# Optimization experiments

Hardware: AMD Instinct MI355X
Metric: run time of the kernel (lower is better)

Reference implementation:

```python
import jax, jax.numpy as jnp
import numpy as np

B, T, D, H, O = 256, 512, 128, 128, 64


def setup_inputs() -> dict:
    key = jax.random.key(0)
    ks = jax.random.split(key, 10)
    s = 1.0 / np.sqrt(H)
    u = lambda k, shape: jax.random.uniform(k, shape, jnp.float32, -s, s)
    return {
        "x": jax.random.normal(ks[0], (B, T, D), jnp.float32),
        "W_ih": u(ks[1], (4 * H, D)),   # torch gate order: i, f, g, o
        "W_hh": u(ks[2], (4 * H, H)),
        "b_ih": u(ks[3], (4 * H,)),
        "b_hh": u(ks[4], (4 * H,)),
        "W1": u(ks[5], (H, H)),
        "b1": u(ks[6], (H,)),
        "W2": u(ks[7], (O, H)),
        "b2": u(ks[8], (O,)),
    }


def lstm_scan(x, W_ih, W_hh, b_ih, b_hh):
    b, t, _ = x.shape
    h4 = W_hh.shape[0] // 4
    # precompute input contribution for all timesteps (one big GEMM)
    xg = jnp.einsum('btd,gd->btg', x, W_ih) + b_ih + b_hh  # (B,T,4H)
    xg = jnp.swapaxes(xg, 0, 1)  # (T,B,4H) for scan over time

    def step(carry, xg_t):
        h, c = carry
        g = xg_t + h @ W_hh.T  # (B,4H)
        i, f, gg, o = jnp.split(g, 4, axis=-1)
        i = jax.nn.sigmoid(i)
        f = jax.nn.sigmoid(f)
        gg = jnp.tanh(gg)
        o = jax.nn.sigmoid(o)
        c = f * c + i * gg
        h = o * jnp.tanh(c)
        return (h, c), h

    h0 = jnp.zeros((b, h4), x.dtype)
    c0 = jnp.zeros((b, h4), x.dtype)
    _, hs = jax.lax.scan(step, (h0, c0), xg)  # hs: (T,B,H)
    return jnp.swapaxes(hs, 0, 1)  # (B,T,H), matching torch batch_first


def reference(x, W_ih, W_hh, b_ih, b_hh, W1, b1, W2, b2):
    b, t, _ = x.shape
    h = lstm_scan(x, W_ih, W_hh, b_ih, b_hh)          # (B,T,H)
    hflat = h.reshape(-1, h.shape[-1])                 # (B*T,H), b-major (as torch)
    hflat = hflat @ W1.T + b1
    y = hflat @ W2.T + b2                              # (B*T,O)
    # faithful to original: reshape flattened b-major rows as (T,B,O), take [-1]
    y = y.reshape(t, b, -1)
    return y[-1]                                       # (B,O)
```

## Files before the change

kernel.cpp:

```cpp
#include <hip/hip_runtime.h>
#include <math.h>

#define BB 256
#define TT 512
#define DD 128
#define HH 128
#define GG 512
#define OO 64

#define LOG2E    1.44269504088896340736f
#define TWOLOG2E 2.88539008177792681472f

typedef _Float16 half8 __attribute__((ext_vector_type(8)));
typedef float    f32x4 __attribute__((ext_vector_type(4)));

__global__ __launch_bounds__(512) void xgpack_kernel(
    const float* __restrict__ x,
    const float* __restrict__ W_ih,
    const float* __restrict__ b_ih,
    const float* __restrict__ b_hh,
    const float* __restrict__ W_hh,
    float* __restrict__ xg,
    _Float16* __restrict__ Wp)
{
    if (blockIdx.x >= TT) {
        const int g = (blockIdx.x - TT) * 512 + threadIdx.x;
        const int fid = g >> 6, l = g & 63;
        const int w = fid >> 5, rem = fid & 31, nt = rem >> 2, kt = rem & 3;
        const int quad = l >> 4, col = l & 15;
        const int row = (nt >> 1) * 128 + (nt & 1) * 16 + w * 32 + col;
        const int off = kt * 32 + quad * 8;
        const float ws = ((row >> 7) == 2) ? TWOLOG2E : LOG2E;
        const float* s = W_hh + row * HH + off;
        _Float16* d = Wp + (size_t)g * 8;
#pragma unroll
        for (int i = 0; i < 8; i++) d[i] = (_Float16)(s[i] * ws);
        return;
    }

    const int t = blockIdx.x;
    const int g = threadIdx.x;

    __shared__ __align__(16) float xs[DD];
    if (g < DD) xs[g] = x[(255 * TT + t) * DD + g];
    __syncthreads();

    const float4* __restrict__ wrow = (const float4*)(W_ih + g * DD);
    const float4* __restrict__ xv   = (const float4*)xs;

    float a0 = 0.f, a1 = 0.f, a2 = 0.f, a3 = 0.f;
#pragma unroll
    for (int i = 0; i < DD / 4; i += 4) {
        float4 w0 = wrow[i + 0], w1 = wrow[i + 1], w2 = wrow[i + 2], w3 = wrow[i + 3];
        float4 h0 = xv[i + 0],  h1 = xv[i + 1],  h2 = xv[i + 2],  h3 = xv[i + 3];
        a0 += w0.x * h0.x + w0.y * h0.y + w0.z * h0.z + w0.w * h0.w;
        a1 += w1.x * h1.x + w1.y * h1.y + w1.z * h1.z + w1.w * h1.w;
        a2 += w2.x * h2.x + w2.y * h2.y + w2.z * h2.z + w2.w * h2.w;
        a3 += w3.x * h3.x + w3.y * h3.y + w3.z * h3.z + w3.w * h3.w;
    }
    const float scale = ((g >> 7) == 2) ? TWOLOG2E : LOG2E;
    const float val = ((a0 + a1) + (a2 + a3) + b_ih[g] + b_hh[g]) * scale;
    xg[t * GG + (g & 127) * 4 + (g >> 7)] = val;
}

__global__
__attribute__((amdgpu_flat_work_group_size(256, 256), amdgpu_waves_per_eu(1, 1)))
void scan_kernel(
    const _Float16* __restrict__ Wp,
    const float* __restrict__ xgp,
    float* __restrict__ hs)
{
    const int tid  = threadIdx.x;
    const int lane = tid & 63;
    const int w    = tid >> 6;
    const int col  = lane & 15;
    const int quad = lane >> 4;
    const int wbase = w * 32;
    const bool sel  = (lane >= 32);
    const int jsel  = wbase + (sel ? 16 : 0) + col;
    const int aoff  = quad * 8;
    const bool wr   = (quad == 0) || (quad == 3);

    __shared__ __align__(16) _Float16 h_lds[2][HH];
    __shared__ __align__(16) float hs_l[BB * HH];

#define BLOADP(nt, kt) \
    half8 B##nt##_##kt = *(const half8*)(Wp + (((w * 32 + (nt) * 4 + (kt)) * 64 + lane) * 8));
#define FOR_KT(X, nt) X(nt, 0) X(nt, 1) X(nt, 2) X(nt, 3)
#define FOR_NT(X) FOR_KT(X, 0) FOR_KT(X, 1) FOR_KT(X, 2) FOR_KT(X, 3) \
                  FOR_KT(X, 4) FOR_KT(X, 5) FOR_KT(X, 6) FOR_KT(X, 7)
    FOR_NT(BLOADP)

    asm volatile("" : "+v"(B0_0), "+v"(B0_1), "+v"(B0_2), "+v"(B0_3),
                      "+v"(B1_0), "+v"(B1_1), "+v"(B1_2), "+v"(B1_3),
                      "+v"(B2_0), "+v"(B2_1), "+v"(B2_2), "+v"(B2_3),
                      "+v"(B3_0), "+v"(B3_1), "+v"(B3_2), "+v"(B3_3));
    asm volatile("" : "+v"(B4_0), "+v"(B4_1), "+v"(B4_2), "+v"(B4_3),
                      "+v"(B5_0), "+v"(B5_1), "+v"(B5_2), "+v"(B5_3),
                      "+v"(B6_0), "+v"(B6_1), "+v"(B6_2), "+v"(B6_3),
                      "+v"(B7_0), "+v"(B7_1), "+v"(B7_2), "+v"(B7_3));

    if (tid < HH) h_lds[0][tid] = (_Float16)0.f;

    f32x4 Z = {0.f, 0.f, 0.f, 0.f};
    asm volatile("" : "+v"(Z));

    const float* __restrict__ xgl = xgp + jsel * 4;
    f32x4 xg0 = *(const f32x4*)(xgl + 0 * GG);
    f32x4 xg1 = *(const f32x4*)(xgl + 1 * GG);

    float c = 0.f;
    __syncthreads();

#define MM(a, b, cc) __builtin_amdgcn_mfma_f32_16x16x32_f16((a), (b), (cc), 0, 0, 0)
#define STEP(par, XCUR) do {                                                            \
    const int t = t2 + (par);                                                           \
    f32x4 xpf = *(const f32x4*)(xgl + ((t + 2) & (TT - 1)) * GG);                       \
    const _Float16* hl = h_lds[(par)];                                                  \
    half8 A0 = *(const half8*)(hl +  0 + aoff);                                         \
    half8 A1 = *(const half8*)(hl + 32 + aoff);                                         \
    half8 A2 = *(const half8*)(hl + 64 + aoff);                                         \
    half8 A3 = *(const half8*)(hl + 96 + aoff);                                         \
    f32x4 C0, C1, C2, C3, C4, C5, C6, C7;                                               \
    C4 = MM(A0, B4_0, Z);  C5 = MM(A0, B5_0, Z);  C0 = MM(A0, B0_0, Z);                 \
    C1 = MM(A0, B1_0, Z);  C2 = MM(A0, B2_0, Z);  C3 = MM(A0, B3_0, Z);                 \
    C6 = MM(A0, B6_0, Z);  C7 = MM(A0, B7_0, Z);                                        \
    C4 = MM(A1, B4_1, C4); C5 = MM(A1, B5_1, C5); C0 = MM(A1, B0_1, C0);                \
    C1 = MM(A1, B1_1, C1); C2 = MM(A1, B2_1, C2); C3 = MM(A1, B3_1, C3);                \
    C6 = MM(A1, B6_1, C6); C7 = MM(A1, B7_1, C7);                                       \
    C4 = MM(A2, B4_2, C4); C5 = MM(A2, B5_2, C5); C0 = MM(A2, B0_2, C0);                \
    C1 = MM(A2, B1_2, C1); C2 = MM(A2, B2_2, C2); C3 = MM(A2, B3_2, C3);                \
    C6 = MM(A2, B6_2, C6); C7 = MM(A2, B7_2, C7);                                       \
    C4 = MM(A3, B4_3, C4); C5 = MM(A3, B5_3, C5); C0 = MM(A3, B0_3, C0);                \
    C1 = MM(A3, B1_3, C1); C2 = MM(A3, B2_3, C2); C3 = MM(A3, B3_3, C3);                \
    C6 = MM(A3, B6_3, C6); C7 = MM(A3, B7_3, C7);                                       \
                   \
    float pi = (sel ? C1[0] : C0[0]) + (XCUR).x;                                        \
    float pf = (sel ? C3[0] : C2[0]) + (XCUR).y;                                        \
    float pg = (sel ? C5[0] : C4[0]) + (XCUR).z;                                        \
    float po = (sel ? C7[0] : C6[0]) + (XCUR).w;                                        \
    float iv = __builtin_amdgcn_rcpf(1.0f + __builtin_amdgcn_exp2f(-pi));               \
    float fv = __builtin_amdgcn_rcpf(1.0f + __builtin_amdgcn_exp2f(-pf));               \
    float ov = __builtin_amdgcn_rcpf(1.0f + __builtin_amdgcn_exp2f(-po));               \
    float Eg = __builtin_amdgcn_exp2f(fabsf(pg));                                       \
    float rg = __builtin_amdgcn_rcpf(Eg + 1.0f);                                        \
    float T  = copysignf(TWOLOG2E, pg);                                                 \
    float gvs = fmaf(-2.0f * T, rg, T);                     \
    c = fmaf(fv, c, iv * gvs);                      \
    float Ec = __builtin_amdgcn_exp2f(fabsf(c));                                        \
    float rc = __builtin_amdgcn_rcpf(Ec + 1.0f);                                        \
    float Ao = copysignf(ov, c);                                                        \
    float hval = fmaf(-2.0f * Ao, rc, Ao);                                              \
    if (wr) {                                                                           \
        h_lds[1 - (par)][jsel] = (_Float16)hval;                                        \
        hs_l[(t & (BB - 1)) * HH + jsel] = hval;          \
    }                                                                                   \
    asm volatile("s_waitcnt lgkmcnt(0)\n\ts_barrier" ::: "memory");                     \
    (XCUR) = xpf;                                                                       \
} while (0)

    for (int t2 = 0; t2 < TT; t2 += 2) {
        STEP(0, xg0);
        STEP(1, xg1);
    }
#undef STEP
#undef MM

    const f32x4* s = (const f32x4*)hs_l;
    f32x4* d = (f32x4*)hs;
#pragma unroll 4
    for (int i = tid; i < BB * HH / 4; i += 256) d[i] = s[i];
}

__global__ __launch_bounds__(128) void mlp_kernel(
    const float* __restrict__ hs,
    const float* __restrict__ W1,
    const float* __restrict__ b1,
    const float* __restrict__ W2,
    const float* __restrict__ b2,
    float* __restrict__ out)
{
    const int r = blockIdx.x;
    const int j = threadIdx.x;

    __shared__ __align__(16) float hsh[HH];
    __shared__ __align__(16) float z[HH];

    hsh[j] = hs[r * HH + j];
    __syncthreads();

    {
        const float4* __restrict__ wrow = (const float4*)(W1 + j * HH);
        const float4* __restrict__ hv   = (const float4*)hsh;
        float acc = b1[j];
#pragma unroll
        for (int i = 0; i < 32; i++) {
            float4 ww = wrow[i], h = hv[i];
            acc += ww.x * h.x + ww.y * h.y + ww.z * h.z + ww.w * h.w;
        }
        z[j] = acc;
    }
    __syncthreads();

    if (j < OO) {
        const float4* __restrict__ wrow = (const float4*)(W2 + j * HH);
        const float4* __restrict__ zv   = (const float4*)z;
        float acc = b2[j];
#pragma unroll
        for (int i = 0; i < 32; i++) {
            float4 ww = wrow[i], zz = zv[i];
            acc += ww.x * zz.x + ww.y * zz.y + ww.z * zz.z + ww.w * zz.w;
        }
        out[r * OO + j] = acc;
    }
}

extern "C" void kernel_launch(void* const* d_in, const int* in_sizes, int n_in,
                              void* d_out, int out_size, void* d_ws, size_t ws_size,
                              hipStream_t stream) {
    const float* x    = (const float*)d_in[0];
    const float* W_ih = (const float*)d_in[1];
    const float* W_hh = (const float*)d_in[2];
    const float* b_ih = (const float*)d_in[3];
    const float* b_hh = (const float*)d_in[4];
    const float* W1   = (const float*)d_in[5];
    const float* b1   = (const float*)d_in[6];
    const float* W2   = (const float*)d_in[7];
    const float* b2   = (const float*)d_in[8];
    float* out = (float*)d_out;

    float*    xg = (float*)d_ws;
    float*    hs = xg + TT * GG;
    _Float16* Wp = (_Float16*)(hs + BB * HH);

    xgpack_kernel<<<TT + 16, 512, 0, stream>>>(x, W_ih, b_ih, b_hh, W_hh, xg, Wp);
    scan_kernel<<<1, 256, 0, stream>>>(Wp, xg, hs);
    mlp_kernel<<<BB, 128, 0, stream>>>(hs, W1, b1, W2, b2, out);
}
```

Baseline: 330.7 us.

## Split recurrent scan across eight waves with one gate tile per wave

Restructures the single-block LSTM scan from 4 waves owning 32 hidden units each to 8 waves owning 16 units each. The W_hh packing layout changes so each wave holds 16 fp16 MFMA B-fragments covering the four gates for its 16 units, instead of 32. This halves the MFMA chain per wave per timestep and removes the lane-half selection. In exchange, each step's barrier now synchronizes twice as many waves, and two waves share each SIMD.

```diff
diff --git a/kernel.cpp b/kernel.cpp
--- a/kernel.cpp
+++ b/kernel.cpp
@@ -26,11 +26,11 @@
     if (blockIdx.x >= TT) {
         const int g = (blockIdx.x - TT) * 512 + threadIdx.x;
         const int fid = g >> 6, l = g & 63;
-        const int w = fid >> 5, rem = fid & 31, nt = rem >> 2, kt = rem & 3;
+        const int w = fid >> 4, rem = fid & 15, gt = rem >> 2, kt = rem & 3;
         const int quad = l >> 4, col = l & 15;
-        const int row = (nt >> 1) * 128 + (nt & 1) * 16 + w * 32 + col;
+        const int row = gt * 128 + w * 16 + col;
         const int off = kt * 32 + quad * 8;
-        const float ws = ((row >> 7) == 2) ? TWOLOG2E : LOG2E;
+        const float ws = (gt == 2) ? TWOLOG2E : LOG2E;
         const float* s = W_hh + row * HH + off;
         _Float16* d = Wp + (size_t)g * 8;
 #pragma unroll
@@ -64,7 +64,7 @@
 }
 
 __global__
-__attribute__((amdgpu_flat_work_group_size(256, 256), amdgpu_waves_per_eu(1, 1)))
+__attribute__((amdgpu_flat_work_group_size(512, 512), amdgpu_waves_per_eu(2, 2)))
 void scan_kernel(
     const _Float16* __restrict__ Wp,
     const float* __restrict__ xgp,
@@ -75,30 +75,23 @@
     const int w    = tid >> 6;
     const int col  = lane & 15;
     const int quad = lane >> 4;
-    const int wbase = w * 32;
-    const bool sel  = (lane >= 32);
-    const int jsel  = wbase + (sel ? 16 : 0) + col;
-    const int aoff  = quad * 8;
-    const bool wr   = (quad == 0) || (quad == 3);
+    const int jsel = w * 16 + col;
+    const int aoff = quad * 8;
+    const bool wr  = (quad == 0);
 
     __shared__ __align__(16) _Float16 h_lds[2][HH];
     __shared__ __align__(16) float hs_l[BB * HH];
 
-#define BLOADP(nt, kt) \
-    half8 B##nt##_##kt = *(const half8*)(Wp + (((w * 32 + (nt) * 4 + (kt)) * 64 + lane) * 8));
-#define FOR_KT(X, nt) X(nt, 0) X(nt, 1) X(nt, 2) X(nt, 3)
-#define FOR_NT(X) FOR_KT(X, 0) FOR_KT(X, 1) FOR_KT(X, 2) FOR_KT(X, 3) \
-                  FOR_KT(X, 4) FOR_KT(X, 5) FOR_KT(X, 6) FOR_KT(X, 7)
-    FOR_NT(BLOADP)
+#define BLOADP(gt, kt) \
+    half8 B##gt##_##kt = *(const half8*)(Wp + (((w * 16 + (gt) * 4 + (kt)) * 64 + lane) * 8));
+#define FOR_KT(X, gt) X(gt, 0) X(gt, 1) X(gt, 2) X(gt, 3)
+#define FOR_GT(X) FOR_KT(X, 0) FOR_KT(X, 1) FOR_KT(X, 2) FOR_KT(X, 3)
+    FOR_GT(BLOADP)
 
     asm volatile("" : "+v"(B0_0), "+v"(B0_1), "+v"(B0_2), "+v"(B0_3),
                       "+v"(B1_0), "+v"(B1_1), "+v"(B1_2), "+v"(B1_3),
                       "+v"(B2_0), "+v"(B2_1), "+v"(B2_2), "+v"(B2_3),
                       "+v"(B3_0), "+v"(B3_1), "+v"(B3_2), "+v"(B3_3));
-    asm volatile("" : "+v"(B4_0), "+v"(B4_1), "+v"(B4_2), "+v"(B4_3),
-                      "+v"(B5_0), "+v"(B5_1), "+v"(B5_2), "+v"(B5_3),
-                      "+v"(B6_0), "+v"(B6_1), "+v"(B6_2), "+v"(B6_3),
-                      "+v"(B7_0), "+v"(B7_1), "+v"(B7_2), "+v"(B7_3));
 
     if (tid < HH) h_lds[0][tid] = (_Float16)0.f;
 
@@ -121,24 +114,20 @@
     half8 A1 = *(const half8*)(hl + 32 + aoff);                                         \
     half8 A2 = *(const half8*)(hl + 64 + aoff);                                         \
     half8 A3 = *(const half8*)(hl + 96 + aoff);                                         \
-    f32x4 C0, C1, C2, C3, C4, C5, C6, C7;                                               \
-    C4 = MM(A0, B4_0, Z);  C5 = MM(A0, B5_0, Z);  C0 = MM(A0, B0_0, Z);                 \
-    C1 = MM(A0, B1_0, Z);  C2 = MM(A0, B2_0, Z);  C3 = MM(A0, B3_0, Z);                 \
-    C6 = MM(A0, B6_0, Z);  C7 = MM(A0, B7_0, Z);                                        \
-    C4 = MM(A1, B4_1, C4); C5 = MM(A1, B5_1, C5); C0 = MM(A1, B0_1, C0);                \
-    C1 = MM(A1, B1_1, C1); C2 = MM(A1, B2_1, C2); C3 = MM(A1, B3_1, C3);                \
-    C6 = MM(A1, B6_1, C6); C7 = MM(A1, B7_1, C7);                                       \
-    C4 = MM(A2, B4_2, C4); C5 = MM(A2, B5_2, C5); C0 = MM(A2, B0_2, C0);                \
-    C1 = MM(A2, B1_2, C1); C2 = MM(A2, B2_2, C2); C3 = MM(A2, B3_2, C3);                \
-    C6 = MM(A2, B6_2, C6); C7 = MM(A2, B7_2, C7);                                       \
-    C4 = MM(A3, B4_3, C4); C5 = MM(A3, B5_3, C5); C0 = MM(A3, B0_3, C0);                \
-    C1 = MM(A3, B1_3, C1); C2 = MM(A3, B2_3, C2); C3 = MM(A3, B3_3, C3);                \
-    C6 = MM(A3, B6_3, C6); C7 = MM(A3, B7_3, C7);                                       \
+    f32x4 C0, C1, C2, C3;                                                               \
+    C0 = MM(A0, B0_0, Z);  C1 = MM(A0, B1_0, Z);                                        \
+    C2 = MM(A0, B2_0, Z);  C3 = MM(A0, B3_0, Z);                                        \
+    C0 = MM(A1, B0_1, C0); C1 = MM(A1, B1_1, C1);                                       \
+    C2 = MM(A1, B2_1, C2); C3 = MM(A1, B3_1, C3);                                       \
+    C0 = MM(A2, B0_2, C0); C1 = MM(A2, B1_2, C1);                                       \
+    C2 = MM(A2, B2_2, C2); C3 = MM(A2, B3_2, C3);                                       \
+    C0 = MM(A3, B0_3, C0); C1 = MM(A3, B1_3, C1);                                       \
+    C2 = MM(A3, B2_3, C2); C3 = MM(A3, B3_3, C3);                                       \
                    \
-    float pi = (sel ? C1[0] : C0[0]) + (XCUR).x;                                        \
-    float pf = (sel ? C3[0] : C2[0]) + (XCUR).y;                                        \
-    float pg = (sel ? C5[0] : C4[0]) + (XCUR).z;                                        \
-    float po = (sel ? C7[0] : C6[0]) + (XCUR).w;                                        \
+    float pi = C0[0] + (XCUR).x;                                                        \
+    float pf = C1[0] + (XCUR).y;                                                        \
+    float pg = C2[0] + (XCUR).z;                                                        \
+    float po = C3[0] + (XCUR).w;                                                        \
     float iv = __builtin_amdgcn_rcpf(1.0f + __builtin_amdgcn_exp2f(-pi));               \
     float fv = __builtin_amdgcn_rcpf(1.0f + __builtin_amdgcn_exp2f(-pf));               \
     float ov = __builtin_amdgcn_rcpf(1.0f + __builtin_amdgcn_exp2f(-po));               \
@@ -169,7 +158,7 @@
     const f32x4* s = (const f32x4*)hs_l;
     f32x4* d = (f32x4*)hs;
 #pragma unroll 4
-    for (int i = tid; i < BB * HH / 4; i += 256) d[i] = s[i];
+    for (int i = tid; i < BB * HH / 4; i += 512) d[i] = s[i];
 }
 
 __global__ __launch_bounds__(128) void mlp_kernel(
@@ -234,6 +223,6 @@
     _Float16* Wp = (_Float16*)(hs + BB * HH);
 
     xgpack_kernel<<<TT + 16, 512, 0, stream>>>(x, W_ih, b_ih, b_hh, W_hh, xg, Wp);
-    scan_kernel<<<1, 256, 0, stream>>>(Wp, xg, hs);
+    scan_kernel<<<1, 512, 0, stream>>>(Wp, xg, hs);
     mlp_kernel<<<BB, 128, 0, stream>>>(hs, W1, b1, W2, b2, out);
 }
```

Result: slower. 349.2 us (+5.6%).
